# Optimization experiments

Hardware: AMD Instinct MI355X
Metric: run time of the kernel (lower is better)

Reference implementation:

```python
import jax, jax.numpy as jnp
import numpy as np

H = 8          # multihead_num (also groups of the Conv1d)
LN_EPS = 1e-5  # torch.nn.LayerNorm default


def _gconv(x, w):
    """Grouped Conv1d, kernel=3, stride=1, 'same' reflect padding, no bias.
    x: [B, C_in, L], w: [C_out, C_in//H, K] (torch OIH layout)."""
    xp = jnp.pad(x, ((0, 0), (0, 0), (1, 1)), mode='reflect')
    return jax.lax.conv_general_dilated(
        xp, w, window_strides=(1,), padding='VALID',
        feature_group_count=H, dimension_numbers=('NCH', 'OIH', 'NCH'))


def setup_inputs() -> dict:
    key = jax.random.key(0)
    ks = jax.random.split(key, 5)
    B, C, L = 8, 512, 1024
    q = jax.random.normal(ks[0], (B, C, L), jnp.float32)
    k = jax.random.normal(ks[1], (B, C, L), jnp.float32)
    # causal mask: 1 above the diagonal -> -1e9 subtracted pre-softmax
    mask = jnp.triu(jnp.ones((L, L), jnp.float32), k=1)
    # init_params: std = sqrt(2 / (C_out + C_in/groups))
    std = float(np.sqrt(2.0 / (C + C // H)))
    wq = jax.random.normal(ks[2], (C, C // H, 3), jnp.float32) * std
    wk = jax.random.normal(ks[3], (C, C // H, 3), jnp.float32) * std
    wv = jax.random.normal(ks[4], (C, C // H, 3), jnp.float32) * std
    gamma = jnp.ones((C,), jnp.float32)
    beta = jnp.zeros((C,), jnp.float32)
    return {"q": q, "k": k, "mask": mask, "wq": wq, "wk": wk, "wv": wv,
            "gamma": gamma, "beta": beta}


def reference(q, k, mask, wq, wk, wv, gamma, beta):
    init = q                               # residual branch, [B, C, L]
    B, C, L = q.shape
    D = C // H                             # head dim
    v = k                                  # inputs list of length 2 -> v = k

    qh = _gconv(q, wq).reshape(B, H, D, L)  # split(dim=1)+cat(dim=0) == head axis
    kh = _gconv(k, wk).reshape(B, H, D, L)
    vh = _gconv(v, wv).reshape(B, H, D, L)

    # scores: q^T k per head; NOTE: scaled by sqrt(multihead_num), as in source
    scores = jnp.einsum('bhdl,bhdm->bhlm', qh, kh) / jnp.sqrt(
        jnp.asarray(H, qh.dtype))
    scores = scores - 1e9 * mask           # mask broadcast over [B, H]
    att = jax.nn.softmax(scores, axis=-1)  # dropout p=0.0 -> identity

    # o = att @ v^T, then concat heads along channel (head-major order)
    o = jnp.einsum('bhlm,bhdm->blhd', att, vh).reshape(B, L, C)

    # residual add + LayerNorm over channel dim
    x = o + jnp.swapaxes(init, 1, 2)       # [B, L, C]
    mu = jnp.mean(x, axis=-1, keepdims=True)
    var = jnp.mean(jnp.square(x - mu), axis=-1, keepdims=True)
    y = (x - mu) * jax.lax.rsqrt(var + LN_EPS) * gamma + beta
    return jnp.swapaxes(y, 1, 2)           # [B, C, L]
```

## Files before the change

kernel.cpp:

```cpp
#include <hip/hip_runtime.h>
#include <math.h>

#define H 8
#define B 8
#define C 512
#define L 1024
#define D 64
#define LDK 72

typedef __attribute__((ext_vector_type(4))) float f32x4;
typedef __attribute__((ext_vector_type(8))) short bf16x8;

static __device__ __forceinline__ short f2bf(float x) {
    union { float f; unsigned u; } v; v.f = x;
    unsigned r = v.u + 0x7FFFu + ((v.u >> 16) & 1u);
    return (short)(r >> 16);
}
static __device__ __forceinline__ int pack2(short a, short b) {
    return (int)((unsigned short)a | ((unsigned)(unsigned short)b << 16));
}

__global__ __launch_bounds__(256) void wprep_kernel(
    const float* __restrict__ wq, const float* __restrict__ wk,
    const float* __restrict__ wv, short* __restrict__ wtg)
{
    int idx = blockIdx.x * 256 + threadIdx.x;
    int jj    = idx & 7;
    int quad  = (idx >> 3) & 3;
    int d     = (idx >> 5) & 63;
    int r     = idx >> 11;
    int khalf = r & 1;  r >>= 1;
    int t     = r % 3;  r /= 3;
    int h     = r & 7;
    int conv  = r >> 3;
    const float* w = (conv == 0) ? wq : (conv == 1) ? wk : wv;
    int j_in = khalf * 32 + quad * 8 + jj;
    wtg[idx] = f2bf(w[(h * 64 + d) * 192 + j_in * 3 + t]);
}

__global__ __launch_bounds__(256) void conv_kernel(
    const float* __restrict__ q, const float* __restrict__ k,
    const short* __restrict__ wtg,
    short* __restrict__ qh, short* __restrict__ kh, short* __restrict__ vh)
{
    int bx   = blockIdx.x;
    int tile = bx & 15;
    int h    = (bx >> 4) & 7;
    int b    = (bx >> 7) & 7;
    int src  = bx >> 10;

    __shared__ short xT[66 * LDK];

    int l0  = tile * 64;
    int tid = threadIdx.x;
    int wave = tid >> 6, lane = tid & 63;
    int n = lane & 15, quad = lane >> 4;

    const float* x  = src ? k : q;
    const float* xb = x + (size_t)(b * C + h * 64) * L + l0;

    int c0 = src ? 1 : 0;
    const short* wb0 = wtg + (size_t)((c0 * 8 + h) * 3 * 2) * 2048;
    bf16x8 wf[3][2], wf2[3][2];
    #pragma unroll
    for (int t = 0; t < 3; t++)
        #pragma unroll
        for (int kk = 0; kk < 2; kk++)
            wf[t][kk] = *(const bf16x8*)(wb0 + (t * 2 + kk) * 2048
                                         + (wave * 16 + n) * 32 + quad * 8);
    if (src) {
        const short* wb1 = wtg + (size_t)((2 * 8 + h) * 3 * 2) * 2048;
        #pragma unroll
        for (int t = 0; t < 3; t++)
            #pragma unroll
            for (int kk = 0; kk < 2; kk++)
                wf2[t][kk] = *(const bf16x8*)(wb1 + (t * 2 + kk) * 2048
                                              + (wave * 16 + n) * 32 + quad * 8);
    }

    {
        int j = tid >> 2;
        #pragma unroll
        for (int s = 0; s < 4; s++) {
            int i = (tid & 3) + s * 4;
            float4 v = *(const float4*)(xb + j * L + i * 4);
            int p = 1 + i * 4;
            xT[(p + 0) * LDK + j] = f2bf(v.x);
            xT[(p + 1) * LDK + j] = f2bf(v.y);
            xT[(p + 2) * LDK + j] = f2bf(v.z);
            xT[(p + 3) * LDK + j] = f2bf(v.w);
        }
        if (tid < 64) {
            int gl = (l0 == 0) ? 1 : (l0 - 1);
            xT[0 * LDK + tid] = f2bf(x[(size_t)(b * C + h * 64 + tid) * L + gl]);
        } else if (tid < 128) {
            int j2 = tid - 64;
            int gl = (l0 + 64 >= L) ? (L - 2) : (l0 + 64);
            xT[65 * LDK + j2] = f2bf(x[(size_t)(b * C + h * 64 + j2) * L + gl]);
        }
    }
    __syncthreads();

    f32x4 acc[4], acc2[4];
    #pragma unroll
    for (int bl = 0; bl < 4; bl++) {
        acc[bl]  = (f32x4){0.f, 0.f, 0.f, 0.f};
        acc2[bl] = (f32x4){0.f, 0.f, 0.f, 0.f};
    }

    #pragma unroll
    for (int bl = 0; bl < 4; bl++) {
        #pragma unroll
        for (int t = 0; t < 3; t++) {
            #pragma unroll
            for (int kk = 0; kk < 2; kk++) {
                bf16x8 bf = *(const bf16x8*)&xT[(bl * 16 + n + t) * LDK
                                                + kk * 32 + quad * 8];
                acc[bl] = __builtin_amdgcn_mfma_f32_16x16x32_bf16(
                    wf[t][kk], bf, acc[bl], 0, 0, 0);
                if (src)
                    acc2[bl] = __builtin_amdgcn_mfma_f32_16x16x32_bf16(
                        wf2[t][kk], bf, acc2[bl], 0, 0, 0);
            }
        }
    }

    int bhh = b * H + h;
    short* o1 = src ? kh : qh;
    {
        short* ob = o1 + ((size_t)bhh * L + l0) * 64;
        #pragma unroll
        for (int bl = 0; bl < 4; bl++) {
            int lg = bl * 16 + n;
            int2 v;
            v.x = pack2(f2bf(acc[bl][0]), f2bf(acc[bl][1]));
            v.y = pack2(f2bf(acc[bl][2]), f2bf(acc[bl][3]));
            *(int2*)&ob[lg * 64 + wave * 16 + quad * 4] = v;
        }
    }
    if (src) {
        short* ob = vh + (size_t)bhh * 64 * L + l0;
        #pragma unroll
        for (int bl = 0; bl < 4; bl++)
            #pragma unroll
            for (int r = 0; r < 4; r++)
                ob[(wave * 16 + quad * 4 + r) * L + bl * 16 + n] = f2bf(acc2[bl][r]);
    }
}

__global__ __launch_bounds__(256, 4) void flash_kernel(
    const short* __restrict__ qh, const short* __restrict__ kh,
    const short* __restrict__ vh, float* __restrict__ o)
{
    int bx = blockIdx.x;
    int bh = bx & 63;
    int qt = 15 - (bx >> 6);
    int h  = bh & 7, b = bh >> 3;

    __shared__ short Qs[64 * LDK];
    __shared__ short Ks[64 * LDK];
    __shared__ short Vt[64 * LDK];
    __shared__ short Ps[64 * LDK];

    int tid  = threadIdx.x;
    int wave = tid >> 6, lane = tid & 63;
    int n    = lane & 15, quad = lane >> 4;

    const short* Qg = qh + ((size_t)bh * L + qt * 64) * 64;
    for (int i = tid; i < 512; i += 256) {
        int row = i >> 3, ch = i & 7;
        *(int4*)&Qs[row * LDK + ch * 8] = ((const int4*)Qg)[i];
    }
    __syncthreads();
    bf16x8 qa0 = *(const bf16x8*)&Qs[(wave * 16 + n) * LDK + quad * 8];
    bf16x8 qa1 = *(const bf16x8*)&Qs[(wave * 16 + n) * LDK + 32 + quad * 8];

    f32x4 O0 = {0.f,0.f,0.f,0.f}, O1 = O0, O2 = O0, O3 = O0;
    float mi[4], li[4];
    #pragma unroll
    for (int r = 0; r < 4; r++) { mi[r] = -INFINITY; li[r] = 0.f; }

    const float scale = 0.35355339059327373f;

    for (int kt = 0; kt <= qt; kt++) {
        __syncthreads();
        const short* Kg = kh + ((size_t)bh * L + kt * 64) * 64;
        const short* Vg = vh + (size_t)bh * 64 * L + kt * 64;
        for (int i = tid; i < 512; i += 256) {
            int row = i >> 3, ch = i & 7;
            *(int4*)&Ks[row * LDK + ch * 8] = ((const int4*)Kg)[i];
            *(int4*)&Vt[row * LDK + ch * 8] = *(const int4*)(Vg + row * (size_t)L + ch * 8);
        }
        __syncthreads();

        f32x4 s[4];
        #pragma unroll
        for (int bk = 0; bk < 4; bk++) {
            bf16x8 kb0 = *(const bf16x8*)&Ks[(bk * 16 + n) * LDK + quad * 8];
            bf16x8 kb1 = *(const bf16x8*)&Ks[(bk * 16 + n) * LDK + 32 + quad * 8];
            f32x4 acc = {0.f,0.f,0.f,0.f};
            acc = __builtin_amdgcn_mfma_f32_16x16x32_bf16(qa0, kb0, acc, 0, 0, 0);
            acc = __builtin_amdgcn_mfma_f32_16x16x32_bf16(qa1, kb1, acc, 0, 0, 0);
            s[bk] = acc;
        }

        #pragma unroll
        for (int bk = 0; bk < 4; bk++)
            #pragma unroll
            for (int r = 0; r < 4; r++) s[bk][r] *= scale;

        if (kt == qt) {
            #pragma unroll
            for (int bk = 0; bk < 4; bk++)
                #pragma unroll
                for (int r = 0; r < 4; r++)
                    if (bk * 16 + n > wave * 16 + quad * 4 + r)
                        s[bk][r] = -INFINITY;
        }

        float rmax[4], rsum[4], alpha[4];
        #pragma unroll
        for (int r = 0; r < 4; r++)
            rmax[r] = fmaxf(fmaxf(s[0][r], s[1][r]), fmaxf(s[2][r], s[3][r]));
        #pragma unroll
        for (int off = 1; off < 16; off <<= 1)
            #pragma unroll
            for (int r = 0; r < 4; r++)
                rmax[r] = fmaxf(rmax[r], __shfl_xor(rmax[r], off, 64));

        #pragma unroll
        for (int r = 0; r < 4; r++) {
            float mnew = fmaxf(mi[r], rmax[r]);
            alpha[r] = __expf(mi[r] - mnew);
            mi[r] = mnew;
            float ls = 0.f;
            #pragma unroll
            for (int bk = 0; bk < 4; bk++) {
                float p = __expf(s[bk][r] - mnew);
                s[bk][r] = p;
                ls += p;
            }
            rsum[r] = ls;
        }
        #pragma unroll
        for (int off = 1; off < 16; off <<= 1)
            #pragma unroll
            for (int r = 0; r < 4; r++)
                rsum[r] += __shfl_xor(rsum[r], off, 64);

        #pragma unroll
        for (int r = 0; r < 4; r++) {
            li[r] = li[r] * alpha[r] + rsum[r];
            O0[r] *= alpha[r]; O1[r] *= alpha[r];
            O2[r] *= alpha[r]; O3[r] *= alpha[r];
        }

        #pragma unroll
        for (int bk = 0; bk < 4; bk++)
            #pragma unroll
            for (int r = 0; r < 4; r++)
                Ps[(wave * 16 + quad * 4 + r) * LDK + bk * 16 + n] = f2bf(s[bk][r]);

        bf16x8 pa0 = *(const bf16x8*)&Ps[(wave * 16 + n) * LDK + quad * 8];
        bf16x8 pa1 = *(const bf16x8*)&Ps[(wave * 16 + n) * LDK + 32 + quad * 8];

        {
            bf16x8 v0, v1;
            v0 = *(const bf16x8*)&Vt[(0 * 16 + n) * LDK + quad * 8];
            v1 = *(const bf16x8*)&Vt[(0 * 16 + n) * LDK + 32 + quad * 8];
            O0 = __builtin_amdgcn_mfma_f32_16x16x32_bf16(pa0, v0, O0, 0, 0, 0);
            O0 = __builtin_amdgcn_mfma_f32_16x16x32_bf16(pa1, v1, O0, 0, 0, 0);
            v0 = *(const bf16x8*)&Vt[(1 * 16 + n) * LDK + quad * 8];
            v1 = *(const bf16x8*)&Vt[(1 * 16 + n) * LDK + 32 + quad * 8];
            O1 = __builtin_amdgcn_mfma_f32_16x16x32_bf16(pa0, v0, O1, 0, 0, 0);
            O1 = __builtin_amdgcn_mfma_f32_16x16x32_bf16(pa1, v1, O1, 0, 0, 0);
            v0 = *(const bf16x8*)&Vt[(2 * 16 + n) * LDK + quad * 8];
            v1 = *(const bf16x8*)&Vt[(2 * 16 + n) * LDK + 32 + quad * 8];
            O2 = __builtin_amdgcn_mfma_f32_16x16x32_bf16(pa0, v0, O2, 0, 0, 0);
            O2 = __builtin_amdgcn_mfma_f32_16x16x32_bf16(pa1, v1, O2, 0, 0, 0);
            v0 = *(const bf16x8*)&Vt[(3 * 16 + n) * LDK + quad * 8];
            v1 = *(const bf16x8*)&Vt[(3 * 16 + n) * LDK + 32 + quad * 8];
            O3 = __builtin_amdgcn_mfma_f32_16x16x32_bf16(pa0, v0, O3, 0, 0, 0);
            O3 = __builtin_amdgcn_mfma_f32_16x16x32_bf16(pa1, v1, O3, 0, 0, 0);
        }
    }

    #pragma unroll
    for (int r = 0; r < 4; r++) {
        float inv = 1.f / li[r];
        int lg = qt * 64 + wave * 16 + quad * 4 + r;
        float* ob = o + ((size_t)b * L + lg) * C + h * 64;
        ob[n]      = O0[r] * inv;
        ob[16 + n] = O1[r] * inv;
        ob[32 + n] = O2[r] * inv;
        ob[48 + n] = O3[r] * inv;
    }
}

__global__ __launch_bounds__(256) void ln_kernel(
    const float* __restrict__ o, const float* __restrict__ q,
    const float* __restrict__ gamma, const float* __restrict__ beta,
    float* __restrict__ y)
{
    int bx = blockIdx.x;
    int tile = bx & 63;
    int b = bx >> 6;
    int l0 = tile * 16;
    int tid = threadIdx.x;

    __shared__ float xt[16 * 516];
    __shared__ float mu_s[16], rs_s[16];

    const float4* og = (const float4*)(o + ((size_t)b * L + l0) * C);
    for (int i = tid; i < 16 * 128; i += 256) {
        int l = i >> 7, c4 = i & 127;
        *(float4*)&xt[l * 516 + c4 * 4] = og[l * 128 + c4];
    }
    __syncthreads();
    const float* qb = q + (size_t)b * C * L + l0;
    for (int i = tid; i < 16 * 512; i += 256) {
        int c = i >> 4, lq = i & 15;
        xt[lq * 516 + c] += qb[c * L + lq];
    }
    __syncthreads();
    {
        int l = tid >> 4, sub = tid & 15;
        float s = 0.f, ss = 0.f;
        for (int j = 0; j < 32; j++) {
            float v = xt[l * 516 + sub + 16 * j];
            s += v; ss += v * v;
        }
        #pragma unroll
        for (int off = 1; off < 16; off <<= 1) {
            s  += __shfl_xor(s, off, 64);
            ss += __shfl_xor(ss, off, 64);
        }
        if (sub == 0) {
            float mean = s * (1.f / 512.f);
            float var  = ss * (1.f / 512.f) - mean * mean;
            mu_s[l] = mean;
            rs_s[l] = rsqrtf(var + 1e-5f);
        }
    }
    __syncthreads();
    float* yb = y + (size_t)b * C * L + l0;
    for (int i = tid; i < 16 * 512; i += 256) {
        int c = i >> 4, lq = i & 15;
        float v = (xt[lq * 516 + c] - mu_s[lq]) * rs_s[lq] * gamma[c] + beta[c];
        yb[c * L + lq] = v;
    }
}

extern "C" void kernel_launch(void* const* d_in, const int* in_sizes, int n_in,
                              void* d_out, int out_size, void* d_ws, size_t ws_size,
                              hipStream_t stream)
{
    const float* q     = (const float*)d_in[0];
    const float* k     = (const float*)d_in[1];
    const float* wq    = (const float*)d_in[3];
    const float* wk    = (const float*)d_in[4];
    const float* wv    = (const float*)d_in[5];
    const float* gamma = (const float*)d_in[6];
    const float* beta  = (const float*)d_in[7];
    float* y = (float*)d_out;

    const size_t N = (size_t)B * H * L * D;
    short* qh  = (short*)d_ws;
    short* kh  = qh + N;
    short* vh  = kh + N;
    float* o   = (float*)(vh + N);
    short* wtg = (short*)(o + (size_t)B * L * C);

    wprep_kernel<<<1152, 256, 0, stream>>>(wq, wk, wv, wtg);
    conv_kernel<<<2 * B * H * (L / 64), 256, 0, stream>>>(q, k, wtg, qh, kh, vh);
    flash_kernel<<<B * H * (L / 64), 256, 0, stream>>>(qh, kh, vh, o);
    ln_kernel<<<B * (L / 16), 256, 0, stream>>>(o, q, gamma, beta, y);
}
```

Before: 157.2 us.

## Process 128 query rows per flash block with register-prefetched K/V and bf16 output

The flash kernel now handles two 64-row query groups per block, so each K/V tile staged in LDS is reused twice. The next K/V tile is prefetched into registers while the current one is computed. The softmax scale and log2(e) are folded into the Q weights so exp2f can replace expf, and the P tile is stored swizzled in the reused Q buffer. The attention output is written as bf16 instead of fp32 to halve that traffic, and the LayerNorm kernel uses vectorized float4 loads and stores. In exchange, occupancy drops to 3 blocks per SM, the grid has half as many blocks, and the extra bf16 rounding reduces precision.

```diff
diff --git a/kernel.cpp b/kernel.cpp
--- a/kernel.cpp
+++ b/kernel.cpp
@@ -16,8 +16,18 @@
     unsigned r = v.u + 0x7FFFu + ((v.u >> 16) & 1u);
     return (short)(r >> 16);
 }
+static __device__ __forceinline__ short f2bf_fast(float x) {
+    union { float f; unsigned u; } v; v.f = x;
+    return (short)((v.u + 0x8000u) >> 16);
+}
 static __device__ __forceinline__ int pack2(short a, short b) {
     return (int)((unsigned short)a | ((unsigned)(unsigned short)b << 16));
+}
+static __device__ __forceinline__ float bf_lo(unsigned u) {
+    union { unsigned u; float f; } v; v.u = u << 16; return v.f;
+}
+static __device__ __forceinline__ float bf_hi(unsigned u) {
+    union { unsigned u; float f; } v; v.u = u & 0xFFFF0000u; return v.f;
 }
 
 __global__ __launch_bounds__(256) void wprep_kernel(
@@ -35,7 +45,9 @@
     int conv  = r >> 3;
     const float* w = (conv == 0) ? wq : (conv == 1) ? wk : wv;
     int j_in = khalf * 32 + quad * 8 + jj;
-    wtg[idx] = f2bf(w[(h * 64 + d) * 192 + j_in * 3 + t]);
+    float v = w[(h * 64 + d) * 192 + j_in * 3 + t];
+    if (conv == 0) v *= 0.51012254f;
+    wtg[idx] = f2bf(v);
 }
 
 __global__ __launch_bounds__(256) void conv_kernel(
@@ -148,157 +160,181 @@
     }
 }
 
-__global__ __launch_bounds__(256, 4) void flash_kernel(
+__global__ __launch_bounds__(256, 3) void flash_kernel(
     const short* __restrict__ qh, const short* __restrict__ kh,
-    const short* __restrict__ vh, float* __restrict__ o)
+    const short* __restrict__ vh, short* __restrict__ o)
 {
-    int bx = blockIdx.x;
-    int bh = bx & 63;
-    int qt = 15 - (bx >> 6);
-    int h  = bh & 7, b = bh >> 3;
-
-    __shared__ short Qs[64 * LDK];
+    int bx  = blockIdx.x;
+    int bh  = bx & 63;
+    int qt2 = 7 - (bx >> 6);
+    int h   = bh & 7, b = bh >> 3;
+
+    __shared__ short QPs[128 * LDK];
     __shared__ short Ks[64 * LDK];
     __shared__ short Vt[64 * LDK];
-    __shared__ short Ps[64 * LDK];
-
-    int tid  = threadIdx.x;
-    int wave = tid >> 6, lane = tid & 63;
-    int n    = lane & 15, quad = lane >> 4;
-
-    const short* Qg = qh + ((size_t)bh * L + qt * 64) * 64;
-    for (int i = tid; i < 512; i += 256) {
+
+    int tid = threadIdx.x, wave = tid >> 6, lane = tid & 63;
+    int n = lane & 15, quad = lane >> 4;
+
+    const short* Qg = qh + ((size_t)bh * L + qt2 * 128) * 64;
+    #pragma unroll
+    for (int jj = 0; jj < 4; jj++) {
+        int i = tid + jj * 256;
         int row = i >> 3, ch = i & 7;
-        *(int4*)&Qs[row * LDK + ch * 8] = ((const int4*)Qg)[i];
-    }
+        *(int4*)&QPs[row * LDK + ch * 8] = ((const int4*)Qg)[i];
+    }
+
+    int ktmax = 2 * qt2 + 2;
+    const short* Kbase = kh + (size_t)bh * L * 64;
+    const short* Vbase = vh + (size_t)bh * 64 * L;
+    int r0 = tid >> 3,         ch0 = tid & 7;
+    int r1 = (tid + 256) >> 3, ch1 = (tid + 256) & 7;
+
+    int4 kreg0, kreg1, vreg0, vreg1;
+    kreg0 = ((const int4*)Kbase)[tid];
+    kreg1 = ((const int4*)Kbase)[tid + 256];
+    vreg0 = *(const int4*)(Vbase + r0 * L + ch0 * 8);
+    vreg1 = *(const int4*)(Vbase + r1 * L + ch1 * 8);
+
     __syncthreads();
-    bf16x8 qa0 = *(const bf16x8*)&Qs[(wave * 16 + n) * LDK + quad * 8];
-    bf16x8 qa1 = *(const bf16x8*)&Qs[(wave * 16 + n) * LDK + 32 + quad * 8];
-
-    f32x4 O0 = {0.f,0.f,0.f,0.f}, O1 = O0, O2 = O0, O3 = O0;
-    float mi[4], li[4];
-    #pragma unroll
-    for (int r = 0; r < 4; r++) { mi[r] = -INFINITY; li[r] = 0.f; }
-
-    const float scale = 0.35355339059327373f;
-
-    for (int kt = 0; kt <= qt; kt++) {
+    bf16x8 qa[2][2];
+    #pragma unroll
+    for (int g = 0; g < 2; g++) {
+        qa[g][0] = *(const bf16x8*)&QPs[(g * 64 + wave * 16 + n) * LDK + quad * 8];
+        qa[g][1] = *(const bf16x8*)&QPs[(g * 64 + wave * 16 + n) * LDK + 32 + quad * 8];
+    }
+
+    f32x4 O[2][4];
+    float mi[2][4], li[2][4];
+    #pragma unroll
+    for (int g = 0; g < 2; g++)
+        #pragma unroll
+        for (int r = 0; r < 4; r++) {
+            O[g][r] = (f32x4){0.f, 0.f, 0.f, 0.f};
+            mi[g][r] = -INFINITY; li[g][r] = 0.f;
+        }
+
+    int swz = ((n >> 2) & 3) << 4;
+
+    for (int kt = 0; kt < ktmax; kt++) {
         __syncthreads();
-        const short* Kg = kh + ((size_t)bh * L + kt * 64) * 64;
-        const short* Vg = vh + (size_t)bh * 64 * L + kt * 64;
-        for (int i = tid; i < 512; i += 256) {
-            int row = i >> 3, ch = i & 7;
-            *(int4*)&Ks[row * LDK + ch * 8] = ((const int4*)Kg)[i];
-            *(int4*)&Vt[row * LDK + ch * 8] = *(const int4*)(Vg + row * (size_t)L + ch * 8);
-        }
+        *(int4*)&Ks[r0 * LDK + ch0 * 8] = kreg0;
+        *(int4*)&Ks[r1 * LDK + ch1 * 8] = kreg1;
+        *(int4*)&Vt[r0 * LDK + ch0 * 8] = vreg0;
+        *(int4*)&Vt[r1 * LDK + ch1 * 8] = vreg1;
         __syncthreads();
-
-        f32x4 s[4];
-        #pragma unroll
-        for (int bk = 0; bk < 4; bk++) {
-            bf16x8 kb0 = *(const bf16x8*)&Ks[(bk * 16 + n) * LDK + quad * 8];
-            bf16x8 kb1 = *(const bf16x8*)&Ks[(bk * 16 + n) * LDK + 32 + quad * 8];
-            f32x4 acc = {0.f,0.f,0.f,0.f};
-            acc = __builtin_amdgcn_mfma_f32_16x16x32_bf16(qa0, kb0, acc, 0, 0, 0);
-            acc = __builtin_amdgcn_mfma_f32_16x16x32_bf16(qa1, kb1, acc, 0, 0, 0);
-            s[bk] = acc;
-        }
-
-        #pragma unroll
-        for (int bk = 0; bk < 4; bk++)
-            #pragma unroll
-            for (int r = 0; r < 4; r++) s[bk][r] *= scale;
-
-        if (kt == qt) {
-            #pragma unroll
-            for (int bk = 0; bk < 4; bk++)
+        if (kt + 1 < ktmax) {
+            const int4* Kg = (const int4*)(Kbase + (size_t)(kt + 1) * 64 * 64);
+            kreg0 = Kg[tid]; kreg1 = Kg[tid + 256];
+            const short* Vg = Vbase + (kt + 1) * 64;
+            vreg0 = *(const int4*)(Vg + r0 * L + ch0 * 8);
+            vreg1 = *(const int4*)(Vg + r1 * L + ch1 * 8);
+        }
+
+        bool lastTile = (kt == ktmax - 1);
+        bool maskTile = (kt == ktmax - 2);
+
+        #pragma unroll
+        for (int g = 0; g < 2; g++) {
+            if (g == 0 && lastTile) continue;
+
+            f32x4 s[4];
+            #pragma unroll
+            for (int bk = 0; bk < 4; bk++) {
+                bf16x8 kb0 = *(const bf16x8*)&Ks[(bk * 16 + n) * LDK + quad * 8];
+                bf16x8 kb1 = *(const bf16x8*)&Ks[(bk * 16 + n) * LDK + 32 + quad * 8];
+                f32x4 acc = {0.f, 0.f, 0.f, 0.f};
+                acc = __builtin_amdgcn_mfma_f32_16x16x32_bf16(qa[g][0], kb0, acc, 0, 0, 0);
+                acc = __builtin_amdgcn_mfma_f32_16x16x32_bf16(qa[g][1], kb1, acc, 0, 0, 0);
+                s[bk] = acc;
+            }
+
+            if ((g == 0 && maskTile) || (g == 1 && lastTile)) {
+                int rowl = wave * 16 + quad * 4;
+                #pragma unroll
+                for (int bk = 0; bk < 4; bk++)
+                    #pragma unroll
+                    for (int r = 0; r < 4; r++)
+                        if (bk * 16 + n > rowl + r) s[bk][r] = -INFINITY;
+            }
+
+            float rmax[4], rsum[4], alpha[4];
+            #pragma unroll
+            for (int r = 0; r < 4; r++)
+                rmax[r] = fmaxf(fmaxf(s[0][r], s[1][r]), fmaxf(s[2][r], s[3][r]));
+            #pragma unroll
+            for (int off = 1; off < 16; off <<= 1)
                 #pragma unroll
                 for (int r = 0; r < 4; r++)
-                    if (bk * 16 + n > wave * 16 + quad * 4 + r)
-                        s[bk][r] = -INFINITY;
-        }
-
-        float rmax[4], rsum[4], alpha[4];
-        #pragma unroll
-        for (int r = 0; r < 4; r++)
-            rmax[r] = fmaxf(fmaxf(s[0][r], s[1][r]), fmaxf(s[2][r], s[3][r]));
-        #pragma unroll
-        for (int off = 1; off < 16; off <<= 1)
-            #pragma unroll
-            for (int r = 0; r < 4; r++)
-                rmax[r] = fmaxf(rmax[r], __shfl_xor(rmax[r], off, 64));
-
+                    rmax[r] = fmaxf(rmax[r], __shfl_xor(rmax[r], off, 64));
+
+            #pragma unroll
+            for (int r = 0; r < 4; r++) {
+                float mnew = fmaxf(mi[g][r], rmax[r]);
+                alpha[r] = exp2f(mi[g][r] - mnew);
+                mi[g][r] = mnew;
+                float ls = 0.f;
+                #pragma unroll
+                for (int bk = 0; bk < 4; bk++) {
+                    float p = exp2f(s[bk][r] - mnew);
+                    s[bk][r] = p;
+                    ls += p;
+                }
+                rsum[r] = ls;
+            }
+            #pragma unroll
+            for (int off = 1; off < 16; off <<= 1)
+                #pragma unroll
+                for (int r = 0; r < 4; r++)
+                    rsum[r] += __shfl_xor(rsum[r], off, 64);
+
+            #pragma unroll
+            for (int r = 0; r < 4; r++) {
+                li[g][r] = li[g][r] * alpha[r] + rsum[r];
+                #pragma unroll
+                for (int bk = 0; bk < 4; bk++) O[g][bk][r] *= alpha[r];
+            }
+
+            #pragma unroll
+            for (int bk = 0; bk < 4; bk++) {
+                int col = ((bk ^ quad) << 4) + n;
+                #pragma unroll
+                for (int r = 0; r < 4; r++)
+                    QPs[(g * 64 + wave * 16 + quad * 4 + r) * LDK + col] =
+                        f2bf_fast(s[bk][r]);
+            }
+
+            bf16x8 pa0 = *(const bf16x8*)&QPs[(g * 64 + wave * 16 + n) * LDK
+                                              + ((quad * 8) ^ swz)];
+            bf16x8 pa1 = *(const bf16x8*)&QPs[(g * 64 + wave * 16 + n) * LDK
+                                              + ((32 + quad * 8) ^ swz)];
+
+            #pragma unroll
+            for (int bk = 0; bk < 4; bk++) {
+                bf16x8 v0 = *(const bf16x8*)&Vt[(bk * 16 + n) * LDK + quad * 8];
+                bf16x8 v1 = *(const bf16x8*)&Vt[(bk * 16 + n) * LDK + 32 + quad * 8];
+                O[g][bk] = __builtin_amdgcn_mfma_f32_16x16x32_bf16(pa0, v0, O[g][bk], 0, 0, 0);
+                O[g][bk] = __builtin_amdgcn_mfma_f32_16x16x32_bf16(pa1, v1, O[g][bk], 0, 0, 0);
+            }
+        }
+    }
+
+    #pragma unroll
+    for (int g = 0; g < 2; g++)
         #pragma unroll
         for (int r = 0; r < 4; r++) {
-            float mnew = fmaxf(mi[r], rmax[r]);
-            alpha[r] = __expf(mi[r] - mnew);
-            mi[r] = mnew;
-            float ls = 0.f;
-            #pragma unroll
-            for (int bk = 0; bk < 4; bk++) {
-                float p = __expf(s[bk][r] - mnew);
-                s[bk][r] = p;
-                ls += p;
-            }
-            rsum[r] = ls;
-        }
-        #pragma unroll
-        for (int off = 1; off < 16; off <<= 1)
-            #pragma unroll
-            for (int r = 0; r < 4; r++)
-                rsum[r] += __shfl_xor(rsum[r], off, 64);
-
-        #pragma unroll
-        for (int r = 0; r < 4; r++) {
-            li[r] = li[r] * alpha[r] + rsum[r];
-            O0[r] *= alpha[r]; O1[r] *= alpha[r];
-            O2[r] *= alpha[r]; O3[r] *= alpha[r];
-        }
-
-        #pragma unroll
-        for (int bk = 0; bk < 4; bk++)
-            #pragma unroll
-            for (int r = 0; r < 4; r++)
-                Ps[(wave * 16 + quad * 4 + r) * LDK + bk * 16 + n] = f2bf(s[bk][r]);
-
-        bf16x8 pa0 = *(const bf16x8*)&Ps[(wave * 16 + n) * LDK + quad * 8];
-        bf16x8 pa1 = *(const bf16x8*)&Ps[(wave * 16 + n) * LDK + 32 + quad * 8];
-
-        {
-            bf16x8 v0, v1;
-            v0 = *(const bf16x8*)&Vt[(0 * 16 + n) * LDK + quad * 8];
-            v1 = *(const bf16x8*)&Vt[(0 * 16 + n) * LDK + 32 + quad * 8];
-            O0 = __builtin_amdgcn_mfma_f32_16x16x32_bf16(pa0, v0, O0, 0, 0, 0);
-            O0 = __builtin_amdgcn_mfma_f32_16x16x32_bf16(pa1, v1, O0, 0, 0, 0);
-            v0 = *(const bf16x8*)&Vt[(1 * 16 + n) * LDK + quad * 8];
-            v1 = *(const bf16x8*)&Vt[(1 * 16 + n) * LDK + 32 + quad * 8];
-            O1 = __builtin_amdgcn_mfma_f32_16x16x32_bf16(pa0, v0, O1, 0, 0, 0);
-            O1 = __builtin_amdgcn_mfma_f32_16x16x32_bf16(pa1, v1, O1, 0, 0, 0);
-            v0 = *(const bf16x8*)&Vt[(2 * 16 + n) * LDK + quad * 8];
-            v1 = *(const bf16x8*)&Vt[(2 * 16 + n) * LDK + 32 + quad * 8];
-            O2 = __builtin_amdgcn_mfma_f32_16x16x32_bf16(pa0, v0, O2, 0, 0, 0);
-            O2 = __builtin_amdgcn_mfma_f32_16x16x32_bf16(pa1, v1, O2, 0, 0, 0);
-            v0 = *(const bf16x8*)&Vt[(3 * 16 + n) * LDK + quad * 8];
-            v1 = *(const bf16x8*)&Vt[(3 * 16 + n) * LDK + 32 + quad * 8];
-            O3 = __builtin_amdgcn_mfma_f32_16x16x32_bf16(pa0, v0, O3, 0, 0, 0);
-            O3 = __builtin_amdgcn_mfma_f32_16x16x32_bf16(pa1, v1, O3, 0, 0, 0);
-        }
-    }
-
-    #pragma unroll
-    for (int r = 0; r < 4; r++) {
-        float inv = 1.f / li[r];
-        int lg = qt * 64 + wave * 16 + quad * 4 + r;
-        float* ob = o + ((size_t)b * L + lg) * C + h * 64;
-        ob[n]      = O0[r] * inv;
-        ob[16 + n] = O1[r] * inv;
-        ob[32 + n] = O2[r] * inv;
-        ob[48 + n] = O3[r] * inv;
-    }
+            float inv = 1.f / li[g][r];
+            int lg = qt2 * 128 + g * 64 + wave * 16 + quad * 4 + r;
+            short* ob = o + ((size_t)b * L + lg) * C + h * 64;
+            ob[n]      = f2bf_fast(O[g][0][r] * inv);
+            ob[16 + n] = f2bf_fast(O[g][1][r] * inv);
+            ob[32 + n] = f2bf_fast(O[g][2][r] * inv);
+            ob[48 + n] = f2bf_fast(O[g][3][r] * inv);
+        }
 }
 
 __global__ __launch_bounds__(256) void ln_kernel(
-    const float* __restrict__ o, const float* __restrict__ q,
+    const short* __restrict__ o, const float* __restrict__ q,
     const float* __restrict__ gamma, const float* __restrict__ beta,
     float* __restrict__ y)
 {
@@ -311,18 +347,33 @@
     __shared__ float xt[16 * 516];
     __shared__ float mu_s[16], rs_s[16];
 
-    const float4* og = (const float4*)(o + ((size_t)b * L + l0) * C);
-    for (int i = tid; i < 16 * 128; i += 256) {
-        int l = i >> 7, c4 = i & 127;
-        *(float4*)&xt[l * 516 + c4 * 4] = og[l * 128 + c4];
+    const int4* og = (const int4*)(o + ((size_t)b * L + l0) * C);
+    #pragma unroll
+    for (int jj = 0; jj < 4; jj++) {
+        int i = tid + jj * 256;
+        int l = i >> 6, c8 = i & 63;
+        int4 v = og[l * 64 + c8];
+        float4 f0, f1;
+        f0.x = bf_lo(v.x); f0.y = bf_hi(v.x); f0.z = bf_lo(v.y); f0.w = bf_hi(v.y);
+        f1.x = bf_lo(v.z); f1.y = bf_hi(v.z); f1.z = bf_lo(v.w); f1.w = bf_hi(v.w);
+        *(float4*)&xt[l * 516 + c8 * 8]     = f0;
+        *(float4*)&xt[l * 516 + c8 * 8 + 4] = f1;
     }
     __syncthreads();
+
     const float* qb = q + (size_t)b * C * L + l0;
-    for (int i = tid; i < 16 * 512; i += 256) {
-        int c = i >> 4, lq = i & 15;
-        xt[lq * 516 + c] += qb[c * L + lq];
+    #pragma unroll
+    for (int jj = 0; jj < 8; jj++) {
+        int i = tid + jj * 256;
+        int c = i >> 2, seg = i & 3;
+        float4 v = *(const float4*)(qb + (size_t)c * L + seg * 4);
+        xt[(seg * 4 + 0) * 516 + c] += v.x;
+        xt[(seg * 4 + 1) * 516 + c] += v.y;
+        xt[(seg * 4 + 2) * 516 + c] += v.z;
+        xt[(seg * 4 + 3) * 516 + c] += v.w;
     }
     __syncthreads();
+
     {
         int l = tid >> 4, sub = tid & 15;
         float s = 0.f, ss = 0.f;
@@ -343,11 +394,19 @@
         }
     }
     __syncthreads();
+
     float* yb = y + (size_t)b * C * L + l0;
-    for (int i = tid; i < 16 * 512; i += 256) {
-        int c = i >> 4, lq = i & 15;
-        float v = (xt[lq * 516 + c] - mu_s[lq]) * rs_s[lq] * gamma[c] + beta[c];
-        yb[c * L + lq] = v;
+    #pragma unroll
+    for (int jj = 0; jj < 8; jj++) {
+        int i = tid + jj * 256;
+        int c = i >> 2, seg = i & 3;
+        float g = gamma[c], be = beta[c];
+        float4 r;
+        r.x = (xt[(seg * 4 + 0) * 516 + c] - mu_s[seg * 4 + 0]) * rs_s[seg * 4 + 0] * g + be;
+        r.y = (xt[(seg * 4 + 1) * 516 + c] - mu_s[seg * 4 + 1]) * rs_s[seg * 4 + 1] * g + be;
+        r.z = (xt[(seg * 4 + 2) * 516 + c] - mu_s[seg * 4 + 2]) * rs_s[seg * 4 + 2] * g + be;
+        r.w = (xt[(seg * 4 + 3) * 516 + c] - mu_s[seg * 4 + 3]) * rs_s[seg * 4 + 3] * g + be;
+        *(float4*)(yb + (size_t)c * L + seg * 4) = r;
     }
 }
 
@@ -368,11 +427,11 @@
     short* qh  = (short*)d_ws;
     short* kh  = qh + N;
     short* vh  = kh + N;
-    float* o   = (float*)(vh + N);
-    short* wtg = (short*)(o + (size_t)B * L * C);
+    short* o   = vh + N;
+    short* wtg = o + N;
 
     wprep_kernel<<<1152, 256, 0, stream>>>(wq, wk, wv, wtg);
     conv_kernel<<<2 * B * H * (L / 64), 256, 0, stream>>>(q, k, wtg, qh, kh, vh);
-    flash_kernel<<<B * H * (L / 64), 256, 0, stream>>>(qh, kh, vh, o);
+    flash_kernel<<<B * H * (L / 128), 256, 0, stream>>>(qh, kh, vh, o);
     ln_kernel<<<B * (L / 16), 256, 0, stream>>>(o, q, gamma, beta, y);
 }
```

After: 169.2 us. 1.08x slower.

## Prefetch K/V in flash loop, fold scale into Wq, bf16 intermediate, coalesce stores

Applied to the files above, without the earlier changes.

Folds the softmax scale and log2(e) into the Q conv weights so the flash loop can use exp2 with no per-element scale. It also prefetches the next K/V tile into registers, and uses a cheaper bf16 rounding for P. The V conv output and the attention output are staged through shared memory so global stores are coalesced, and the attention output becomes bf16 instead of fp32. LayerNorm is retiled to 4 rows per block with vectorized loads and stores. Storing the attention output in bf16 adds rounding error before the residual and LayerNorm.

```diff
diff --git a/kernel.cpp b/kernel.cpp
--- a/kernel.cpp
+++ b/kernel.cpp
@@ -16,8 +16,18 @@
     unsigned r = v.u + 0x7FFFu + ((v.u >> 16) & 1u);
     return (short)(r >> 16);
 }
+static __device__ __forceinline__ short f2bf_fast(float x) {
+    union { float f; unsigned u; } v; v.f = x;
+    return (short)((v.u + 0x8000u) >> 16);
+}
 static __device__ __forceinline__ int pack2(short a, short b) {
     return (int)((unsigned short)a | ((unsigned)(unsigned short)b << 16));
+}
+static __device__ __forceinline__ float bf_lo(unsigned u) {
+    union { unsigned u; float f; } v; v.u = u << 16; return v.f;
+}
+static __device__ __forceinline__ float bf_hi(unsigned u) {
+    union { unsigned u; float f; } v; v.u = u & 0xFFFF0000u; return v.f;
 }
 
 __global__ __launch_bounds__(256) void wprep_kernel(
@@ -35,7 +45,9 @@
     int conv  = r >> 3;
     const float* w = (conv == 0) ? wq : (conv == 1) ? wk : wv;
     int j_in = khalf * 32 + quad * 8 + jj;
-    wtg[idx] = f2bf(w[(h * 64 + d) * 192 + j_in * 3 + t]);
+    float v = w[(h * 64 + d) * 192 + j_in * 3 + t];
+    if (conv == 0) v *= 0.51012254f;
+    wtg[idx] = f2bf(v);
 }
 
 __global__ __launch_bounds__(256) void conv_kernel(
@@ -139,18 +151,28 @@
         }
     }
     if (src) {
-        short* ob = vh + (size_t)bhh * 64 * L + l0;
+        __syncthreads();
         #pragma unroll
         for (int bl = 0; bl < 4; bl++)
             #pragma unroll
             for (int r = 0; r < 4; r++)
-                ob[(wave * 16 + quad * 4 + r) * L + bl * 16 + n] = f2bf(acc2[bl][r]);
+                xT[(wave * 16 + quad * 4 + r) * LDK + bl * 16 + n] =
+                    f2bf(acc2[bl][r]);
+        __syncthreads();
+        short* vb = vh + (size_t)bhh * 64 * L + l0;
+        #pragma unroll
+        for (int jj = 0; jj < 2; jj++) {
+            int i = tid + jj * 256;
+            int row = i >> 3, seg = i & 7;
+            int4 v = *(const int4*)&xT[row * LDK + seg * 8];
+            *(int4*)(vb + (size_t)row * L + seg * 8) = v;
+        }
     }
 }
 
 __global__ __launch_bounds__(256, 4) void flash_kernel(
     const short* __restrict__ qh, const short* __restrict__ kh,
-    const short* __restrict__ vh, float* __restrict__ o)
+    const short* __restrict__ vh, short* __restrict__ o)
 {
     int bx = blockIdx.x;
     int bh = bx & 63;
@@ -171,6 +193,17 @@
         int row = i >> 3, ch = i & 7;
         *(int4*)&Qs[row * LDK + ch * 8] = ((const int4*)Qg)[i];
     }
+
+    const short* Kbase = kh + (size_t)bh * L * 64;
+    const short* Vbase = vh + (size_t)bh * 64 * L;
+    int r0 = tid >> 3,         ch0 = tid & 7;
+    int r1 = (tid + 256) >> 3, ch1 = (tid + 256) & 7;
+
+    int4 kreg0 = ((const int4*)Kbase)[tid];
+    int4 kreg1 = ((const int4*)Kbase)[tid + 256];
+    int4 vreg0 = *(const int4*)(Vbase + r0 * L + ch0 * 8);
+    int4 vreg1 = *(const int4*)(Vbase + r1 * L + ch1 * 8);
+
     __syncthreads();
     bf16x8 qa0 = *(const bf16x8*)&Qs[(wave * 16 + n) * LDK + quad * 8];
     bf16x8 qa1 = *(const bf16x8*)&Qs[(wave * 16 + n) * LDK + 32 + quad * 8];
@@ -180,18 +213,20 @@
     #pragma unroll
     for (int r = 0; r < 4; r++) { mi[r] = -INFINITY; li[r] = 0.f; }
 
-    const float scale = 0.35355339059327373f;
-
     for (int kt = 0; kt <= qt; kt++) {
         __syncthreads();
-        const short* Kg = kh + ((size_t)bh * L + kt * 64) * 64;
-        const short* Vg = vh + (size_t)bh * 64 * L + kt * 64;
-        for (int i = tid; i < 512; i += 256) {
-            int row = i >> 3, ch = i & 7;
-            *(int4*)&Ks[row * LDK + ch * 8] = ((const int4*)Kg)[i];
-            *(int4*)&Vt[row * LDK + ch * 8] = *(const int4*)(Vg + row * (size_t)L + ch * 8);
-        }
+        *(int4*)&Ks[r0 * LDK + ch0 * 8] = kreg0;
+        *(int4*)&Ks[r1 * LDK + ch1 * 8] = kreg1;
+        *(int4*)&Vt[r0 * LDK + ch0 * 8] = vreg0;
+        *(int4*)&Vt[r1 * LDK + ch1 * 8] = vreg1;
         __syncthreads();
+        if (kt < qt) {
+            const int4* Kg = (const int4*)(Kbase + (size_t)(kt + 1) * 64 * 64);
+            kreg0 = Kg[tid]; kreg1 = Kg[tid + 256];
+            const short* Vg = Vbase + (kt + 1) * 64;
+            vreg0 = *(const int4*)(Vg + r0 * L + ch0 * 8);
+            vreg1 = *(const int4*)(Vg + r1 * L + ch1 * 8);
+        }
 
         f32x4 s[4];
         #pragma unroll
@@ -204,11 +239,6 @@
             s[bk] = acc;
         }
 
-        #pragma unroll
-        for (int bk = 0; bk < 4; bk++)
-            #pragma unroll
-            for (int r = 0; r < 4; r++) s[bk][r] *= scale;
-
         if (kt == qt) {
             #pragma unroll
             for (int bk = 0; bk < 4; bk++)
@@ -231,12 +261,12 @@
         #pragma unroll
         for (int r = 0; r < 4; r++) {
             float mnew = fmaxf(mi[r], rmax[r]);
-            alpha[r] = __expf(mi[r] - mnew);
+            alpha[r] = exp2f(mi[r] - mnew);
             mi[r] = mnew;
             float ls = 0.f;
             #pragma unroll
             for (int bk = 0; bk < 4; bk++) {
-                float p = __expf(s[bk][r] - mnew);
+                float p = exp2f(s[bk][r] - mnew);
                 s[bk][r] = p;
                 ls += p;
             }
@@ -259,95 +289,113 @@
         for (int bk = 0; bk < 4; bk++)
             #pragma unroll
             for (int r = 0; r < 4; r++)
-                Ps[(wave * 16 + quad * 4 + r) * LDK + bk * 16 + n] = f2bf(s[bk][r]);
+                Ps[(wave * 16 + quad * 4 + r) * LDK + bk * 16 + n] =
+                    f2bf_fast(s[bk][r]);
 
         bf16x8 pa0 = *(const bf16x8*)&Ps[(wave * 16 + n) * LDK + quad * 8];
         bf16x8 pa1 = *(const bf16x8*)&Ps[(wave * 16 + n) * LDK + 32 + quad * 8];
 
-        {
-            bf16x8 v0, v1;
-            v0 = *(const bf16x8*)&Vt[(0 * 16 + n) * LDK + quad * 8];
-            v1 = *(const bf16x8*)&Vt[(0 * 16 + n) * LDK + 32 + quad * 8];
-            O0 = __builtin_amdgcn_mfma_f32_16x16x32_bf16(pa0, v0, O0, 0, 0, 0);
-            O0 = __builtin_amdgcn_mfma_f32_16x16x32_bf16(pa1, v1, O0, 0, 0, 0);
-            v0 = *(const bf16x8*)&Vt[(1 * 16 + n) * LDK + quad * 8];
-            v1 = *(const bf16x8*)&Vt[(1 * 16 + n) * LDK + 32 + quad * 8];
-            O1 = __builtin_amdgcn_mfma_f32_16x16x32_bf16(pa0, v0, O1, 0, 0, 0);
-            O1 = __builtin_amdgcn_mfma_f32_16x16x32_bf16(pa1, v1, O1, 0, 0, 0);
-            v0 = *(const bf16x8*)&Vt[(2 * 16 + n) * LDK + quad * 8];
-            v1 = *(const bf16x8*)&Vt[(2 * 16 + n) * LDK + 32 + quad * 8];
-            O2 = __builtin_amdgcn_mfma_f32_16x16x32_bf16(pa0, v0, O2, 0, 0, 0);
-            O2 = __builtin_amdgcn_mfma_f32_16x16x32_bf16(pa1, v1, O2, 0, 0, 0);
-            v0 = *(const bf16x8*)&Vt[(3 * 16 + n) * LDK + quad * 8];
-            v1 = *(const bf16x8*)&Vt[(3 * 16 + n) * LDK + 32 + quad * 8];
-            O3 = __builtin_amdgcn_mfma_f32_16x16x32_bf16(pa0, v0, O3, 0, 0, 0);
-            O3 = __builtin_amdgcn_mfma_f32_16x16x32_bf16(pa1, v1, O3, 0, 0, 0);
-        }
-    }
-
+        #pragma unroll
+        for (int bk = 0; bk < 4; bk++) {
+            bf16x8 v0 = *(const bf16x8*)&Vt[(bk * 16 + n) * LDK + quad * 8];
+            bf16x8 v1 = *(const bf16x8*)&Vt[(bk * 16 + n) * LDK + 32 + quad * 8];
+            f32x4* Op = (bk == 0) ? &O0 : (bk == 1) ? &O1 : (bk == 2) ? &O2 : &O3;
+            *Op = __builtin_amdgcn_mfma_f32_16x16x32_bf16(pa0, v0, *Op, 0, 0, 0);
+            *Op = __builtin_amdgcn_mfma_f32_16x16x32_bf16(pa1, v1, *Op, 0, 0, 0);
+        }
+    }
+
+    __syncthreads();
     #pragma unroll
     for (int r = 0; r < 4; r++) {
         float inv = 1.f / li[r];
-        int lg = qt * 64 + wave * 16 + quad * 4 + r;
-        float* ob = o + ((size_t)b * L + lg) * C + h * 64;
-        ob[n]      = O0[r] * inv;
-        ob[16 + n] = O1[r] * inv;
-        ob[32 + n] = O2[r] * inv;
-        ob[48 + n] = O3[r] * inv;
+        int rowl = wave * 16 + quad * 4 + r;
+        Ks[rowl * LDK + n]      = f2bf_fast(O0[r] * inv);
+        Ks[rowl * LDK + 16 + n] = f2bf_fast(O1[r] * inv);
+        Ks[rowl * LDK + 32 + n] = f2bf_fast(O2[r] * inv);
+        Ks[rowl * LDK + 48 + n] = f2bf_fast(O3[r] * inv);
+    }
+    __syncthreads();
+    #pragma unroll
+    for (int jj = 0; jj < 2; jj++) {
+        int i = tid + jj * 256;
+        int row = i >> 3, seg = i & 7;
+        int4 v = *(const int4*)&Ks[row * LDK + seg * 8];
+        *(int4*)(o + ((size_t)(b * L + qt * 64 + row)) * C + h * 64 + seg * 8) = v;
     }
 }
 
 __global__ __launch_bounds__(256) void ln_kernel(
-    const float* __restrict__ o, const float* __restrict__ q,
+    const short* __restrict__ o, const float* __restrict__ q,
     const float* __restrict__ gamma, const float* __restrict__ beta,
     float* __restrict__ y)
 {
     int bx = blockIdx.x;
-    int tile = bx & 63;
-    int b = bx >> 6;
-    int l0 = tile * 16;
+    int tile = bx & 255;
+    int b = bx >> 8;
+    int l0 = tile * 4;
     int tid = threadIdx.x;
 
-    __shared__ float xt[16 * 516];
-    __shared__ float mu_s[16], rs_s[16];
-
-    const float4* og = (const float4*)(o + ((size_t)b * L + l0) * C);
-    for (int i = tid; i < 16 * 128; i += 256) {
-        int l = i >> 7, c4 = i & 127;
-        *(float4*)&xt[l * 516 + c4 * 4] = og[l * 128 + c4];
-    }
-    __syncthreads();
+    __shared__ float xt[4 * 516];
+    __shared__ float mu_s[4], rs_s[4];
+
+    {
+        const int4* og = (const int4*)(o + ((size_t)b * L + l0) * C);
+        int l = tid >> 6, c8 = tid & 63;
+        int4 v = og[tid];
+        float4 f0, f1;
+        f0.x = bf_lo(v.x); f0.y = bf_hi(v.x); f0.z = bf_lo(v.y); f0.w = bf_hi(v.y);
+        f1.x = bf_lo(v.z); f1.y = bf_hi(v.z); f1.z = bf_lo(v.w); f1.w = bf_hi(v.w);
+        *(float4*)&xt[l * 516 + c8 * 8]     = f0;
+        *(float4*)&xt[l * 516 + c8 * 8 + 4] = f1;
+    }
+    __syncthreads();
+
     const float* qb = q + (size_t)b * C * L + l0;
-    for (int i = tid; i < 16 * 512; i += 256) {
-        int c = i >> 4, lq = i & 15;
-        xt[lq * 516 + c] += qb[c * L + lq];
-    }
-    __syncthreads();
+    #pragma unroll
+    for (int jj = 0; jj < 2; jj++) {
+        int c = tid + jj * 256;
+        float4 v = *(const float4*)(qb + (size_t)c * L);
+        xt[0 * 516 + c] += v.x;
+        xt[1 * 516 + c] += v.y;
+        xt[2 * 516 + c] += v.z;
+        xt[3 * 516 + c] += v.w;
+    }
+    __syncthreads();
+
     {
-        int l = tid >> 4, sub = tid & 15;
+        int w = tid >> 6, lanei = tid & 63;
         float s = 0.f, ss = 0.f;
-        for (int j = 0; j < 32; j++) {
-            float v = xt[l * 516 + sub + 16 * j];
+        #pragma unroll
+        for (int j = 0; j < 8; j++) {
+            float v = xt[w * 516 + lanei + 64 * j];
             s += v; ss += v * v;
         }
         #pragma unroll
-        for (int off = 1; off < 16; off <<= 1) {
+        for (int off = 1; off < 64; off <<= 1) {
             s  += __shfl_xor(s, off, 64);
             ss += __shfl_xor(ss, off, 64);
         }
-        if (sub == 0) {
+        if (lanei == 0) {
             float mean = s * (1.f / 512.f);
             float var  = ss * (1.f / 512.f) - mean * mean;
-            mu_s[l] = mean;
-            rs_s[l] = rsqrtf(var + 1e-5f);
-        }
-    }
-    __syncthreads();
+            mu_s[w] = mean;
+            rs_s[w] = rsqrtf(var + 1e-5f);
+        }
+    }
+    __syncthreads();
+
     float* yb = y + (size_t)b * C * L + l0;
-    for (int i = tid; i < 16 * 512; i += 256) {
-        int c = i >> 4, lq = i & 15;
-        float v = (xt[lq * 516 + c] - mu_s[lq]) * rs_s[lq] * gamma[c] + beta[c];
-        yb[c * L + lq] = v;
+    #pragma unroll
+    for (int jj = 0; jj < 2; jj++) {
+        int c = tid + jj * 256;
+        float g = gamma[c], be = beta[c];
+        float4 r;
+        r.x = (xt[0 * 516 + c] - mu_s[0]) * rs_s[0] * g + be;
+        r.y = (xt[1 * 516 + c] - mu_s[1]) * rs_s[1] * g + be;
+        r.z = (xt[2 * 516 + c] - mu_s[2]) * rs_s[2] * g + be;
+        r.w = (xt[3 * 516 + c] - mu_s[3]) * rs_s[3] * g + be;
+        *(float4*)(yb + (size_t)c * L) = r;
     }
 }
 
@@ -368,11 +416,11 @@
     short* qh  = (short*)d_ws;
     short* kh  = qh + N;
     short* vh  = kh + N;
-    float* o   = (float*)(vh + N);
-    short* wtg = (short*)(o + (size_t)B * L * C);
+    short* o   = vh + N;
+    short* wtg = o + N;
 
     wprep_kernel<<<1152, 256, 0, stream>>>(wq, wk, wv, wtg);
     conv_kernel<<<2 * B * H * (L / 64), 256, 0, stream>>>(q, k, wtg, qh, kh, vh);
     flash_kernel<<<B * H * (L / 64), 256, 0, stream>>>(qh, kh, vh, o);
-    ln_kernel<<<B * (L / 16), 256, 0, stream>>>(o, q, gamma, beta, y);
-}
+    ln_kernel<<<B * (L / 4), 256, 0, stream>>>(o, q, gamma, beta, y);
+}
```

After: 179.6 us. 1.14x slower.
